# Optimization experiments

Measured on AMD Instinct MI355X. Metric: run time of the kernel, lower is better.

Reference implementation:

```python
import jax, jax.numpy as jnp
import numpy as np

EMBED_DIM = 1024
NUM_HEADS = 16
HEAD_DIM = EMBED_DIM // NUM_HEADS


def setup_inputs() -> dict:
    key = jax.random.key(0)
    ks = jax.random.split(key, 5)
    B, S, D = 2, 2048, EMBED_DIM
    scale = 1.0 / np.sqrt(D)
    x = jax.random.normal(ks[0], (B, S, D), dtype=jnp.float32)
    qkv_w = jax.random.uniform(ks[1], (3 * D, D), dtype=jnp.float32, minval=-scale, maxval=scale)
    qkv_b = jax.random.uniform(ks[2], (3 * D,), dtype=jnp.float32, minval=-scale, maxval=scale)
    out_w = jax.random.uniform(ks[3], (D, D), dtype=jnp.float32, minval=-scale, maxval=scale)
    out_b = jax.random.uniform(ks[4], (D,), dtype=jnp.float32, minval=-scale, maxval=scale)
    return {"x": x, "qkv_w": qkv_w, "qkv_b": qkv_b, "out_w": out_w, "out_b": out_b}


def reference(x, qkv_w, qkv_b, out_w, out_b):
    B, S, D = x.shape
    H, hd = NUM_HEADS, HEAD_DIM
    # QKV projection (torch Linear: y = x @ W^T + b)
    qkv = jnp.einsum('bsd,ed->bse', x, qkv_w) + qkv_b          # [B,S,3D]
    qkv = qkv.reshape(B, S, 3, H, hd)
    q, k, v = (jnp.moveaxis(qkv[:, :, i], 2, 1) for i in range(3))  # each [B,H,S,hd]
    scores = jnp.einsum('bhqd,bhkd->bhqk', q, k) / np.sqrt(hd)  # [B,H,S,S]
    probs = jax.nn.softmax(scores, axis=-1)
    attn = jnp.einsum('bhqk,bhkd->bhqd', probs, v)              # [B,H,S,hd]
    attn = jnp.moveaxis(attn, 1, 2).reshape(B, S, D)
    return jnp.einsum('bsd,ed->bse', attn, out_w) + out_b
```

## Files before the change

### kernel.cpp

```cpp
#include <hip/hip_runtime.h>
#include <stdint.h>

typedef __bf16 bf16;
typedef __attribute__((ext_vector_type(2))) __bf16 bf16x2;
typedef __attribute__((ext_vector_type(4))) __bf16 bf16x4;
typedef __attribute__((ext_vector_type(8))) __bf16 bf16x8;
typedef __attribute__((ext_vector_type(4))) float f32x4;
typedef __attribute__((ext_vector_type(16))) float f32x16;

#define LOG2E_OVER_8 0.18033688011112042f

#if __has_builtin(__builtin_amdgcn_exp2f)
#define EXP2(x) __builtin_amdgcn_exp2f(x)
#else
#define EXP2(x) exp2f(x)
#endif

__device__ __forceinline__ void gl_lds16(const bf16* g, bf16* l) {
  __builtin_amdgcn_global_load_lds(
      (const __attribute__((address_space(1))) void*)g,
      (__attribute__((address_space(3))) void*)l, 16, 0, 0);
}
#define WAIT_VM0_BARRIER() asm volatile("s_waitcnt vmcnt(0)\n\ts_barrier" ::: "memory")

__device__ __forceinline__ uint32_t pack2(float a, float b) {
  union { bf16x2 v; uint32_t u; } z;
  z.v[0] = (bf16)a; z.v[1] = (bf16)b;
  return z.u;
}

__device__ __forceinline__ void pl32swap(uint32_t& a, uint32_t& b) {
  asm("v_permlane32_swap_b32 %0, %1" : "+v"(a), "+v"(b));
}

#define N_X  (4096 * 1024)
#define N_WQ (3072 * 1024)
#define N_WO (1024 * 1024)
__global__ __launch_bounds__(256) void cvt3_kernel(const float* __restrict__ x,
                                                   const float* __restrict__ wq,
                                                   const float* __restrict__ wo,
                                                   bf16* __restrict__ d) {
  int i = (blockIdx.x * 256 + threadIdx.x) * 8;
  const float* s;
  if (i < N_X) s = x + i;
  else if (i < N_X + N_WQ) s = wq + (i - N_X);
  else s = wo + (i - N_X - N_WQ);
  float4 a = *(const float4*)s;
  float4 b = *(const float4*)(s + 4);
  bf16x8 o;
  o[0] = (bf16)a.x; o[1] = (bf16)a.y; o[2] = (bf16)a.z; o[3] = (bf16)a.w;
  o[4] = (bf16)b.x; o[5] = (bf16)b.y; o[6] = (bf16)b.z; o[7] = (bf16)b.w;
  *(bf16x8*)(d + i) = o;
}

template <int EPI>
__global__ __launch_bounds__(256, 3) void gemm_bt(
    const bf16* __restrict__ A, const bf16* __restrict__ Bw,
    const float* __restrict__ bias,
    bf16* __restrict__ qo, bf16* __restrict__ ko, bf16* __restrict__ vTo,
    float* __restrict__ outF) {
  constexpr int MT = EPI ? 64 : 128;
  constexpr int MI = MT / 32;
  constexpr int BK = EPI ? 64 : 32;
  constexpr int NC = BK / 32;
  constexpr int NIT = 1024 / BK;
  constexpr int ASZ = MT * BK;
  constexpr int BSZ = 128 * BK;
  constexpr int RS = 136;
  constexpr int SME0 = 2 * ASZ + 2 * BSZ;
  constexpr int SME = EPI ? SME0 : (SME0 > 128 * RS ? SME0 : 128 * RS);
  __shared__ __attribute__((aligned(16))) bf16 smem[SME];

  int bx, by;
  {
    const int f = blockIdx.x;
    const int xcd = f & 7, idx = f >> 3;
    if constexpr (EPI == 0) { by = xcd * 4 + (idx & 3); bx = idx >> 2; }
    else                    { by = xcd * 8 + (idx & 7); bx = idx >> 3; }
  }

  const int t = threadIdx.x;
  const int L = t & 63;
  const int li = L & 15;
  const int qd = L >> 4;
  const int w = t >> 6;
  const int wm = (w >> 1) * (MT / 2);
  const int wn = (w & 1) * 64;
  const int bm0 = by * MT;
  const int bn0 = bx * 128;
  const int r_st = t >> 2;
  const int c_st = (t & 3) * 8;

  const bf16* Ab = A + (size_t)bm0 * 1024;
  const bf16* Bb = Bw + (size_t)bn0 * 1024;

  auto issue = [&](int k0, int bi) {
    bf16* As_ = smem + bi * ASZ;
    bf16* Bs_ = smem + 2 * ASZ + bi * BSZ;
#pragma unroll
    for (int kc = 0; kc < NC; ++kc) {
      const int kk = k0 + kc * 32;
      gl_lds16(Ab + (size_t)r_st * 1024 + kk + c_st, As_ + kc * MT * 32 + t * 8);
      if constexpr (MT == 128)
        gl_lds16(Ab + (size_t)(r_st + 64) * 1024 + kk + c_st,
                 As_ + kc * MT * 32 + (t + 256) * 8);
      gl_lds16(Bb + (size_t)r_st * 1024 + kk + c_st, Bs_ + kc * 4096 + t * 8);
      gl_lds16(Bb + (size_t)(r_st + 64) * 1024 + kk + c_st,
               Bs_ + kc * 4096 + (t + 256) * 8);
    }
  };

  f32x4 acc[MI][4] = {};
  issue(0, 0);
  for (int it = 0; it < NIT; ++it) {
    WAIT_VM0_BARRIER();
    if (it < NIT - 1) issue((it + 1) * BK, (it + 1) & 1);
    const bf16* Ac = smem + (it & 1) * ASZ;
    const bf16* Bc = smem + 2 * ASZ + (it & 1) * BSZ;
#pragma unroll
    for (int kc = 0; kc < NC; ++kc) {
      const bf16* Ak = Ac + kc * MT * 32;
      const bf16* Bk = Bc + kc * 4096;
      bf16x8 af[MI], bfr[4];
#pragma unroll
      for (int mi = 0; mi < MI; ++mi)
        af[mi] = *(const bf16x8*)(Ak + (wm + mi * 16 + li) * 32 + qd * 8);
#pragma unroll
      for (int ni = 0; ni < 4; ++ni)
        bfr[ni] = *(const bf16x8*)(Bk + (wn + ni * 16 + li) * 32 + qd * 8);
#pragma unroll
      for (int mi = 0; mi < MI; ++mi)
#pragma unroll
        for (int ni = 0; ni < 4; ++ni)
          acc[mi][ni] = __builtin_amdgcn_mfma_f32_16x16x32_bf16(
              af[mi], bfr[ni], acc[mi][ni], 0, 0, 0);
    }
  }

  if constexpr (EPI == 0) {
    const int which = bn0 >> 10;
    __syncthreads();
    bf16* Ct = smem;
    if (which == 2) {
#pragma unroll
      for (int mi = 0; mi < MI; ++mi) {
        const int m_l = wm + mi * 16 + qd * 4;
#pragma unroll
        for (int ni = 0; ni < 4; ++ni) {
          const int n_l = wn + ni * 16 + li;
          const float bi = bias[bn0 + n_l];
          bf16x4 pk;
#pragma unroll
          for (int r = 0; r < 4; ++r) pk[r] = (bf16)(acc[mi][ni][r] + bi);
          *(bf16x4*)(Ct + n_l * RS + m_l) = pk;
        }
      }
    } else {
      const float sc = (which == 0) ? LOG2E_OVER_8 : 1.0f;
#pragma unroll
      for (int mi = 0; mi < MI; ++mi) {
        const int m_l = wm + mi * 16 + qd * 4;
#pragma unroll
        for (int ni = 0; ni < 4; ++ni) {
          const int n_l = wn + ni * 16 + li;
          const float bi = bias[bn0 + n_l];
#pragma unroll
          for (int r = 0; r < 4; ++r)
            Ct[(m_l + r) * RS + n_l] = (bf16)((acc[mi][ni][r] + bi) * sc);
        }
      }
    }
    __syncthreads();
    const int jr = t >> 4;
    const int jc = t & 15;
#pragma unroll
    for (int pass = 0; pass < 8; ++pass) {
      const int row = pass * 16 + jr;
      bf16x8 vv = *(const bf16x8*)(Ct + row * RS + jc * 8);
      if (which == 2) {
        const int n_g = bn0 + row;
        const int hh = (n_g >> 6) & 15, dd = n_g & 63;
        const int bb = bm0 >> 11;
        const int s_b = (bm0 & 2047) + jc * 8;
        *(bf16x8*)(vTo + ((size_t)(bb * 16 + hh) * 64 + dd) * 2048 + s_b) = vv;
      } else {
        const int m_g = bm0 + row;
        const int bb = m_g >> 11, ss = m_g & 2047;
        const int n_g = bn0 + jc * 8;
        const int hh = (n_g >> 6) & 15, dd = n_g & 63;
        bf16* dst = (which == 0 ? qo : ko);
        *(bf16x8*)(dst + ((size_t)(bb * 16 + hh) * 2048 + ss) * 64 + dd) = vv;
      }
    }
  } else {
#pragma unroll
    for (int mi = 0; mi < MI; ++mi) {
      const int m_g = bm0 + wm + mi * 16 + qd * 4;
#pragma unroll
      for (int ni = 0; ni < 4; ++ni) {
        const int n_g = bn0 + wn + ni * 16 + li;
        const float bi = bias[n_g];
#pragma unroll
        for (int r = 0; r < 4; ++r)
          outF[(size_t)(m_g + r) * 1024 + n_g] = acc[mi][ni][r] + bi;
      }
    }
  }
}

__global__ __launch_bounds__(256, 2) void attn_fwd(
    const bf16* __restrict__ Q, const bf16* __restrict__ K,
    const bf16* __restrict__ VT, bf16* __restrict__ AO) {
  __shared__ __attribute__((aligned(16))) bf16 Ks[2 * 8192];
  __shared__ __attribute__((aligned(16))) bf16 Vs[2 * 8192];
  const int t = threadIdx.x;
  const int L = t & 63;
  const int m31 = L & 31;
  const int hi = L >> 5;
  const int w = t >> 6;

  const int lid = blockIdx.x;
  const int bh_ = ((lid & 7) << 2) + (lid >> 7);
  const int qb = (lid >> 3) & 15;
  const int b = bh_ >> 4, h = bh_ & 15;
  const size_t bh = (size_t)(b * 16 + h);

  const bf16* Qp = Q + bh * 2048 * 64;
  const bf16* Kp = K + bh * 2048 * 64;
  const bf16* Vp = VT + bh * 64 * 2048;
  const int q0 = qb * 128 + w * 32;

  bf16x8 qf[4];
#pragma unroll
  for (int s = 0; s < 4; ++s)
    qf[s] = *(const bf16x8*)(Qp + (size_t)(q0 + m31) * 64 + s * 16 + hi * 8);

  f32x16 acc[2][2] = {};
  float ls[4] = {0.f, 0.f, 0.f, 0.f};

  const int srow = t >> 3;
  const int scc = (t & 7) ^ (srow & 7);
  auto issue = [&](int it2, int bi) {
#pragma unroll
    for (int tile = 0; tile < 2; ++tile) {
      const int kt = it2 * 2 + tile;
      const bf16* Kt = Kp + (size_t)kt * 4096;
      const bf16* Vt = Vp + kt * 64;
      bf16* Kd = Ks + bi * 8192 + tile * 4096;
      bf16* Vd = Vs + bi * 8192 + tile * 4096;
#pragma unroll
      for (int r = 0; r < 2; ++r) {
        gl_lds16(Kt + (srow + 32 * r) * 64 + scc * 8, Kd + (t + 256 * r) * 8);
        gl_lds16(Vt + (size_t)(srow + 32 * r) * 2048 + scc * 8, Vd + (t + 256 * r) * 8);
      }
    }
  };

  const int rlow = m31 & 7;
  issue(0, 0);
  for (int it2 = 0; it2 < 16; ++it2) {
    WAIT_VM0_BARRIER();
    if (it2 < 15) issue(it2 + 1, (it2 + 1) & 1);
    const bf16* Kc0 = Ks + (it2 & 1) * 8192;
    const bf16* Vc0 = Vs + (it2 & 1) * 8192;

    f32x16 st[2][2];
#pragma unroll
    for (int tile = 0; tile < 2; ++tile) {
      const bf16* Kc = Kc0 + tile * 4096;
#pragma unroll
      for (int kt2 = 0; kt2 < 2; ++kt2) {
        f32x16 z = {};
#pragma unroll
        for (int s = 0; s < 4; ++s) {
          bf16x8 kf = *(const bf16x8*)(
              Kc + ((kt2 * 32 + m31) * 8 + ((2 * s + hi) ^ rlow)) * 8);
          z = __builtin_amdgcn_mfma_f32_32x32x16_bf16(kf, qf[s], z, 0, 0, 0);
        }
        st[tile][kt2] = z;
      }
    }

    union FU { uint32_t u[4]; bf16x8 v; };
    FU af[2][2][2];
#pragma unroll
    for (int tile = 0; tile < 2; ++tile)
#pragma unroll
      for (int kt2 = 0; kt2 < 2; ++kt2) {
        uint32_t pk[8];
        float lsl = 0.f;
#pragma unroll
        for (int j = 0; j < 8; ++j) {
          float a = EXP2(st[tile][kt2][2 * j]);
          float c = EXP2(st[tile][kt2][2 * j + 1]);
          lsl += a + c;
          pk[j] = pack2(a, c);
        }
        ls[tile * 2 + kt2] += lsl;
        pl32swap(pk[0], pk[2]);
        pl32swap(pk[1], pk[3]);
        pl32swap(pk[4], pk[6]);
        pl32swap(pk[5], pk[7]);
        af[tile][kt2][0].u[0] = pk[0]; af[tile][kt2][0].u[1] = pk[1];
        af[tile][kt2][0].u[2] = pk[2]; af[tile][kt2][0].u[3] = pk[3];
        af[tile][kt2][1].u[0] = pk[4]; af[tile][kt2][1].u[1] = pk[5];
        af[tile][kt2][1].u[2] = pk[6]; af[tile][kt2][1].u[3] = pk[7];
      }

#pragma unroll
    for (int dt = 0; dt < 2; ++dt)
#pragma unroll
      for (int tile = 0; tile < 2; ++tile) {
        const bf16* Vc = Vc0 + tile * 4096;
#pragma unroll
        for (int kt2 = 0; kt2 < 2; ++kt2)
#pragma unroll
          for (int u = 0; u < 2; ++u) {
            bf16x8 vf = *(const bf16x8*)(
                Vc + ((dt * 32 + m31) * 8 + ((kt2 * 4 + u * 2 + hi) ^ rlow)) * 8);
            acc[dt][tile] = __builtin_amdgcn_mfma_f32_32x32x16_bf16(
                af[tile][kt2][u].v, vf, acc[dt][tile], 0, 0, 0);
          }
      }
  }

  f32x16 accf[2];
#pragma unroll
  for (int dt = 0; dt < 2; ++dt) accf[dt] = acc[dt][0] + acc[dt][1];
  float lsum = (ls[0] + ls[1]) + (ls[2] + ls[3]);
  lsum += __shfl_xor(lsum, 32);
  const float inv = 1.f / lsum;

#pragma unroll
  for (int r = 0; r < 16; ++r) {
    const int qrow = (r & 3) + 8 * (r >> 2) + 4 * hi;
    const float invq = __shfl(inv, qrow);
    const size_t base = ((size_t)b * 2048 + q0 + qrow) * 1024 + h * 64 + m31;
    AO[base] = (bf16)(accf[0][r] * invq);
    AO[base + 32] = (bf16)(accf[1][r] * invq);
  }
}

extern "C" void kernel_launch(void* const* d_in, const int* in_sizes, int n_in,
                              void* d_out, int out_size, void* d_ws, size_t ws_size,
                              hipStream_t stream) {
  const float* x = (const float*)d_in[0];
  const float* qkvw = (const float*)d_in[1];
  const float* qkvb = (const float*)d_in[2];
  const float* outw = (const float*)d_in[3];
  const float* outb = (const float*)d_in[4];
  float* out = (float*)d_out;

  bf16* xb = (bf16*)d_ws;
  bf16* wq = xb + (size_t)N_X;
  bf16* wo = wq + (size_t)N_WQ;
  bf16* q = wo + (size_t)N_WO;
  bf16* kk = q + (size_t)2 * 16 * 2048 * 64;
  bf16* vT = kk + (size_t)2 * 16 * 2048 * 64;
  bf16* attn = xb;

  cvt3_kernel<<<4096, 256, 0, stream>>>(x, qkvw, outw, xb);

  gemm_bt<0><<<768, 256, 0, stream>>>(xb, wq, qkvb, q, kk, vT, nullptr);
  attn_fwd<<<512, 256, 0, stream>>>(q, kk, vT, attn);
  gemm_bt<1><<<512, 256, 0, stream>>>(attn, wo, outb, nullptr, nullptr, nullptr, out);
}
```

Baseline: 176.5 us.

## Triple-buffer QKV GEMM loads and split K/V prefetch in attention

The QKV projection GEMM moves from double to triple buffering in LDS. It keeps two tiles in flight and waits with vmcnt(4) instead of draining all loads each iteration. The attention kernel splits K and V prefetch into separate issue stages, waiting only for K before the QK^T MFMAs and for V before PV, so loads overlap compute more finely. This costs more LDS in the GEMM, which may reduce occupancy, and adds an extra barrier per attention iteration.

```diff
diff --git a/kernel.cpp b/kernel.cpp
--- a/kernel.cpp
+++ b/kernel.cpp
@@ -22,6 +22,7 @@
       (__attribute__((address_space(3))) void*)l, 16, 0, 0);
 }
 #define WAIT_VM0_BARRIER() asm volatile("s_waitcnt vmcnt(0)\n\ts_barrier" ::: "memory")
+#define WAIT_VM4_BARRIER() asm volatile("s_waitcnt vmcnt(4)\n\ts_barrier" ::: "memory")
 
 __device__ __forceinline__ uint32_t pack2(float a, float b) {
   union { bf16x2 v; uint32_t u; } z;
@@ -66,8 +67,9 @@
   constexpr int NIT = 1024 / BK;
   constexpr int ASZ = MT * BK;
   constexpr int BSZ = 128 * BK;
+  constexpr int NBUF = EPI ? 2 : 3;
   constexpr int RS = 136;
-  constexpr int SME0 = 2 * ASZ + 2 * BSZ;
+  constexpr int SME0 = NBUF * ASZ + NBUF * BSZ;
   constexpr int SME = EPI ? SME0 : (SME0 > 128 * RS ? SME0 : 128 * RS);
   __shared__ __attribute__((aligned(16))) bf16 smem[SME];
 
@@ -96,7 +98,7 @@
 
   auto issue = [&](int k0, int bi) {
     bf16* As_ = smem + bi * ASZ;
-    bf16* Bs_ = smem + 2 * ASZ + bi * BSZ;
+    bf16* Bs_ = smem + NBUF * ASZ + bi * BSZ;
 #pragma unroll
     for (int kc = 0; kc < NC; ++kc) {
       const int kk = k0 + kc * 32;
@@ -111,12 +113,8 @@
   };
 
   f32x4 acc[MI][4] = {};
-  issue(0, 0);
-  for (int it = 0; it < NIT; ++it) {
-    WAIT_VM0_BARRIER();
-    if (it < NIT - 1) issue((it + 1) * BK, (it + 1) & 1);
-    const bf16* Ac = smem + (it & 1) * ASZ;
-    const bf16* Bc = smem + 2 * ASZ + (it & 1) * BSZ;
+
+  auto compute_tile = [&](const bf16* Ac, const bf16* Bc) {
 #pragma unroll
     for (int kc = 0; kc < NC; ++kc) {
       const bf16* Ak = Ac + kc * MT * 32;
@@ -134,6 +132,24 @@
         for (int ni = 0; ni < 4; ++ni)
           acc[mi][ni] = __builtin_amdgcn_mfma_f32_16x16x32_bf16(
               af[mi], bfr[ni], acc[mi][ni], 0, 0, 0);
+    }
+  };
+
+  if constexpr (EPI == 0) {
+    issue(0, 0);
+    issue(BK, 1);
+    for (int it = 0; it < NIT; ++it) {
+      if (it < NIT - 1) WAIT_VM4_BARRIER();
+      else              WAIT_VM0_BARRIER();
+      if (it < NIT - 2) issue((it + 2) * BK, (it + 2) % 3);
+      compute_tile(smem + (it % 3) * ASZ, smem + NBUF * ASZ + (it % 3) * BSZ);
+    }
+  } else {
+    issue(0, 0);
+    for (int it = 0; it < NIT; ++it) {
+      WAIT_VM0_BARRIER();
+      if (it < NIT - 1) issue((it + 1) * BK, (it + 1) & 1);
+      compute_tile(smem + (it & 1) * ASZ, smem + NBUF * ASZ + (it & 1) * BSZ);
     }
   }
 
@@ -240,27 +256,34 @@
 
   const int srow = t >> 3;
   const int scc = (t & 7) ^ (srow & 7);
-  auto issue = [&](int it2, int bi) {
+  auto issueK = [&](int it2, int bi) {
 #pragma unroll
     for (int tile = 0; tile < 2; ++tile) {
       const int kt = it2 * 2 + tile;
       const bf16* Kt = Kp + (size_t)kt * 4096;
+      bf16* Kd = Ks + bi * 8192 + tile * 4096;
+#pragma unroll
+      for (int r = 0; r < 2; ++r)
+        gl_lds16(Kt + (srow + 32 * r) * 64 + scc * 8, Kd + (t + 256 * r) * 8);
+    }
+  };
+  auto issueV = [&](int it2, int bi) {
+#pragma unroll
+    for (int tile = 0; tile < 2; ++tile) {
+      const int kt = it2 * 2 + tile;
       const bf16* Vt = Vp + kt * 64;
-      bf16* Kd = Ks + bi * 8192 + tile * 4096;
       bf16* Vd = Vs + bi * 8192 + tile * 4096;
 #pragma unroll
-      for (int r = 0; r < 2; ++r) {
-        gl_lds16(Kt + (srow + 32 * r) * 64 + scc * 8, Kd + (t + 256 * r) * 8);
+      for (int r = 0; r < 2; ++r)
         gl_lds16(Vt + (size_t)(srow + 32 * r) * 2048 + scc * 8, Vd + (t + 256 * r) * 8);
-      }
     }
   };
 
   const int rlow = m31 & 7;
-  issue(0, 0);
+  issueK(0, 0);
+  issueV(0, 0);
   for (int it2 = 0; it2 < 16; ++it2) {
-    WAIT_VM0_BARRIER();
-    if (it2 < 15) issue(it2 + 1, (it2 + 1) & 1);
+    WAIT_VM4_BARRIER();
     const bf16* Kc0 = Ks + (it2 & 1) * 8192;
     const bf16* Vc0 = Vs + (it2 & 1) * 8192;
 
@@ -280,6 +303,13 @@
         st[tile][kt2] = z;
       }
     }
+
+    if (it2 < 15) issueK(it2 + 1, (it2 + 1) & 1);
+
+    if (it2 < 15) WAIT_VM4_BARRIER();
+    else          WAIT_VM0_BARRIER();
+
+    if (it2 < 15) issueV(it2 + 1, (it2 + 1) & 1);
 
     union FU { uint32_t u[4]; bf16x8 v; };
     FU af[2][2][2];
```

After: 178.2 us. About the same (+1.0%).
